# Kernel tuning notes

Hardware: AMD Instinct MI355X
Metric: run time of the kernel (lower is better)

Reference implementation:

```python
import jax, jax.numpy as jnp
import numpy as np

S, B, W, H = 97, 256, 1024, 16
HD = W // H


def setup_inputs() -> dict:
    key = jax.random.key(0)
    ks = jax.random.split(key, 16)
    def p(k, shape):
        return jax.random.normal(k, shape, jnp.float32) * 0.02
    return {
        "tensor": jax.random.normal(ks[0], (S, B, W), jnp.float32),
        "mask": jnp.zeros((S, S), jnp.float32),
        "q_w": p(ks[1], (W, W)), "q_b": p(ks[2], (W,)),
        "k_w": p(ks[3], (W, W)), "k_b": p(ks[4], (W,)),
        "v_w": p(ks[5], (W, W)), "v_b": p(ks[6], (W,)),
        "in_proj_w": p(ks[7], (3 * W, W)), "in_proj_b": p(ks[8], (3 * W,)),
        "mha_out_w": p(ks[9], (W, W)), "mha_out_b": p(ks[10], (W,)),
        "out_w": p(ks[11], (W, W)), "out_b": p(ks[12], (W,)),
    }


def _freqs_cos_sin(dim, seqlen, theta=10000.0):
    # matches precompute_freqs_cis: angle[t, j] = t / theta**(2j/dim)
    inv = 1.0 / (theta ** (jnp.arange(0, dim, 2, dtype=jnp.float32) / dim))  # (dim/2,)
    ang = jnp.arange(seqlen, dtype=jnp.float32)[:, None] * inv[None, :]      # (S, dim/2)
    return jnp.cos(ang)[:, None, :], jnp.sin(ang)[:, None, :]                # (S, 1, dim/2)


def _rotary(x, cos, sin):
    # x: (S, B, D); pairs (even, odd) along last dim form complex numbers
    s, b, d = x.shape
    xr = x.reshape(s, b, d // 2, 2)
    xe, xo = xr[..., 0], xr[..., 1]
    oe = xe * cos - xo * sin
    oo = xe * sin + xo * cos
    return jnp.stack([oe, oo], axis=-1).reshape(s, b, d)


def reference(tensor, mask, q_w, q_b, k_w, k_b, v_w, v_b,
              in_proj_w, in_proj_b, mha_out_w, mha_out_b, out_w, out_b):
    # tensor: (S, B, W) -- torch MHA default batch_first=False layout
    q = tensor @ q_w.T + q_b
    k = tensor @ k_w.T + k_b
    v = tensor @ v_w.T + v_b

    cos, sin = _freqs_cos_sin(W, S)
    q = _rotary(q, cos, sin)
    k = _rotary(k, cos, sin)

    # nn.MultiheadAttention internal in_proj (applied on top of q/k/v linears)
    Wq, Wk, Wv = in_proj_w[:W], in_proj_w[W:2 * W], in_proj_w[2 * W:]
    bq, bk, bv = in_proj_b[:W], in_proj_b[W:2 * W], in_proj_b[2 * W:]
    q = q @ Wq.T + bq
    k = k @ Wk.T + bk
    v = v @ Wv.T + bv

    def split_heads(x):  # (S,B,W) -> (B,H,S,HD)
        return x.reshape(S, B, H, HD).transpose(1, 2, 0, 3)

    qh, kh, vh = split_heads(q), split_heads(k), split_heads(v)
    scale = 1.0 / jnp.sqrt(jnp.float32(HD))
    scores = jnp.einsum('bhqd,bhkd->bhqk', qh, kh) * scale + mask  # additive float mask
    attn = jax.nn.softmax(scores, axis=-1)
    o = jnp.einsum('bhqk,bhkd->bhqd', attn, vh)      # (B,H,S,HD)
    o = o.transpose(2, 0, 1, 3).reshape(S, B, W)     # (S,B,W)
    o = o @ mha_out_w.T + mha_out_b                  # MHA out_proj
    return o @ out_w.T + out_b                       # module's final self.out
```

## Files before the change

### kernel.cpp

```cpp
#include <hip/hip_runtime.h>
#include <cstdint>
#include <cstddef>

#define S_LEN 97
#define B_DIM 256
#define W_DIM 1024
#define NH    16
#define HDIM  64
#define MROWS (S_LEN * B_DIM)

typedef unsigned short u16;
typedef __bf16 bf16x8 __attribute__((ext_vector_type(8)));
typedef float  f32x4  __attribute__((ext_vector_type(4)));

__device__ __forceinline__ u16 f2bf(float f) {
  __bf16 b = (__bf16)f;
  return __builtin_bit_cast(unsigned short, b);
}

__device__ __forceinline__ void gload16(const void* g, void* lds) {
  __builtin_amdgcn_global_load_lds(
      (const __attribute__((address_space(1))) void*)(uintptr_t)g,
      (__attribute__((address_space(3))) void*)(uint32_t)(uintptr_t)lds,
      16, 0, 0);
}

__global__ void k_prep(const float* __restrict__ tensor, u16* __restrict__ Xbf,
                       const float* __restrict__ q_w, const float* __restrict__ k_w,
                       const float* __restrict__ in_proj_w, const float* __restrict__ out_w,
                       u16* __restrict__ WC1, u16* __restrict__ W2, u16* __restrict__ WO,
                       const float* __restrict__ v_w, u16* __restrict__ WvT,
                       const float* __restrict__ mha_w, u16* __restrict__ WmT,
                       const float* __restrict__ v_b, const float* __restrict__ in_proj_b,
                       float* __restrict__ bvf,
                       const float* __restrict__ mha_b, const float* __restrict__ out_b,
                       float* __restrict__ bff,
                       float* __restrict__ tab, const float* __restrict__ mask,
                       float* __restrict__ maskP, const float* __restrict__ q_b,
                       const float* __restrict__ k_b, float* __restrict__ bc1,
                       float* __restrict__ zb) {
  __shared__ float tlds[32][33];
  const int blk = blockIdx.x, t = threadIdx.x;

  if (blk < 24832) {
    const int i = blk * 256 + t;
    float4 v = ((const float4*)tensor)[i];
    uint2 pk;
    pk.x = (uint32_t)f2bf(v.x) | ((uint32_t)f2bf(v.y) << 16);
    pk.y = (uint32_t)f2bf(v.z) | ((uint32_t)f2bf(v.w) << 16);
    ((uint2*)Xbf)[i] = pk;
  } else if (blk < 30976) {
    const int i = (blk - 24832) * 256 + t;
    const float* s; u16* d; int off;
    if (i < 262144)        { s = q_w;       d = WC1;           off = i; }
    else if (i < 524288)   { s = k_w;       d = WC1 + 1048576; off = i - 262144; }
    else if (i < 1310720)  { s = in_proj_w; d = W2;            off = i - 524288; }
    else                   { s = out_w;     d = WO;            off = i - 1310720; }
    float4 v = ((const float4*)s)[off];
    uint2 pk;
    pk.x = (uint32_t)f2bf(v.x) | ((uint32_t)f2bf(v.y) << 16);
    pk.y = (uint32_t)f2bf(v.z) | ((uint32_t)f2bf(v.w) << 16);
    ((uint2*)d)[off] = pk;
  } else if (blk < 33024) {
    const int idx = blk - 30976;
    const int z = idx >> 10, rem = idx & 1023;
    const float* src = z ? mha_w : v_w;
    u16* dst = z ? WmT : WvT;
    const int bx = (rem & 31) * 32, by = (rem >> 5) * 32;
    const int tx = t & 31, ty = t >> 5;
    for (int yy = ty; yy < 32; yy += 8)
      tlds[yy][tx] = src[(size_t)(by + yy) * 1024 + bx + tx];
    __syncthreads();
    for (int yy = ty; yy < 32; yy += 8)
      dst[(size_t)(bx + yy) * 1024 + by + tx] = f2bf(tlds[tx][yy]);
  } else if (blk < 33536) {
    const int bb = blk - 33024;
    const int lane = t & 63, wave = t >> 6;
    const float* M; const float* v; const float* b2; float* out; int rb;
    if (bb < 256) { M = in_proj_w + (size_t)2048 * 1024; v = v_b; b2 = in_proj_b + 2048; out = bvf; rb = bb * 4; }
    else          { M = out_w; v = mha_b; b2 = out_b; out = bff; rb = (bb - 256) * 4; }
    const int row = rb + wave;
    float s = 0.f;
    for (int k = lane; k < 1024; k += 64) s += M[(size_t)row * 1024 + k] * v[k];
#pragma unroll
    for (int d = 32; d; d >>= 1) s += __shfl_xor(s, d);
    if (lane == 0) out[row] = s + b2[row];
  } else {
    const int bb = blk - 33536;
    if (bb < 194) {
      const int idx = bb * 256 + t;
      if (idx < S_LEN * 512) {
        const int s = idx / 512, i = idx % 512;
        const float freq = expf(-(float)i * (9.210340371976184f / 512.0f));
        float sv, cv;
        sincosf((float)s * freq, &sv, &cv);
        tab[idx * 2 + 0] = cv;
        tab[idx * 2 + 1] = sv;
      }
    } else if (bb < 258) {
      const int i = (bb - 194) * 256 + t;
      const int r = i >> 7, c = i & 127;
      float v;
      if (c >= S_LEN) v = -1e30f;
      else if (r < S_LEN) v = mask[r * S_LEN + c];
      else v = 0.f;
      maskP[i] = v;
    } else if (bb < 266) {
      const int i = (bb - 258) * 256 + t;
      bc1[i] = (i < W_DIM) ? q_b[i] : k_b[i - W_DIM];
    } else {
      const int i = (bb - 266) * 256 + t;
      zb[i] = 0.f;
    }
  }
}

__global__ __launch_bounds__(256) void k_gemmfold(
    const u16* __restrict__ A0, const u16* __restrict__ B0, u16* __restrict__ C0,
    const u16* __restrict__ A1, const u16* __restrict__ B1, u16* __restrict__ C1,
    const float* __restrict__ zb) {
  __shared__ u16 As[128 * 64];
  __shared__ u16 Bs[128 * 64];

  const u16* A = blockIdx.z ? A1 : A0;
  const u16* Bw = blockIdx.z ? B1 : B0;
  u16* Cp = blockIdx.z ? C1 : C0;

  const int tid = threadIdx.x, lane = tid & 63, wave = tid >> 6;
  const int wm = wave >> 1, wn = wave & 1;
  const int m0 = blockIdx.y * 128;
  const int n0 = blockIdx.x * 128;

  f32x4 acc[4][4] = {};

  const int lrow = lane >> 3;
  const int lcol = (lane & 7) * 8;
  const u16* Ag = A + (size_t)(m0 + wave * 8 + lrow) * 1024 + lcol;
  const u16* Bg = Bw + (size_t)(n0 + wave * 8 + lrow) * 1024 + lcol;
  u16* Asl = As + wave * 8 * 64;
  u16* Bsl = Bs + wave * 8 * 64;

  for (int kt = 0; kt < 1024; kt += 64) {
#pragma unroll
    for (int i = 0; i < 4; ++i) {
      gload16(Ag + (size_t)(i * 32) * 1024 + kt, Asl + i * 2048);
      gload16(Bg + (size_t)(i * 32) * 1024 + kt, Bsl + i * 2048);
    }
    __syncthreads();
#pragma unroll
    for (int kk = 0; kk < 2; ++kk) {
      bf16x8 af[4], bfr[4];
#pragma unroll
      for (int m = 0; m < 4; ++m)
        af[m] = *(const bf16x8*)(As + (wm * 64 + m * 16 + (lane & 15)) * 64 + kk * 32 + (lane >> 4) * 8);
#pragma unroll
      for (int n = 0; n < 4; ++n)
        bfr[n] = *(const bf16x8*)(Bs + (wn * 64 + n * 16 + (lane & 15)) * 64 + kk * 32 + (lane >> 4) * 8);
#pragma unroll
      for (int m = 0; m < 4; ++m)
#pragma unroll
        for (int n = 0; n < 4; ++n)
          acc[m][n] = __builtin_amdgcn_mfma_f32_16x16x32_bf16(af[m], bfr[n], acc[m][n], 0, 0, 0);
    }
    __syncthreads();
  }

  const int r0 = (lane >> 4) * 4;
  const int c0 = lane & 15;
#pragma unroll
  for (int m = 0; m < 4; ++m)
#pragma unroll
    for (int n = 0; n < 4; ++n) {
      const int col = n0 + wn * 64 + n * 16 + c0;
#pragma unroll
      for (int r = 0; r < 4; ++r) {
        const int row = m0 + wm * 64 + m * 16 + r0 + r;
        Cp[(size_t)row * 1024 + col] = f2bf(acc[m][n][r] + zb[col]);
      }
    }
}

template <int MODE>
__global__ __launch_bounds__(512, 4) void k_gemm256(
    const u16* __restrict__ A, int lda,
    const u16* __restrict__ BwA, const u16* __restrict__ BwB,
    const float* __restrict__ biasA, const float* __restrict__ biasB,
    void* __restrict__ CpA, void* __restrict__ CpB, int ldc,
    size_t thirdStride, const float* __restrict__ tab, int Nt, int NtA) {
  __shared__ u16 lds[3 * 12288];

  const int tid = threadIdx.x, lane = tid & 63, wave = tid >> 6;
  const int wm = wave >> 2, wn = wave & 3;
  const int c0 = lane & 15, hi = lane >> 4;

  const int nwg = gridDim.x;
  const int qq = nwg >> 3, rr_ = nwg & 7;
  const int xcd = blockIdx.x & 7, sub = blockIdx.x >> 3;
  const int seq = (xcd < rr_ ? xcd * (qq + 1) : rr_ * (qq + 1) + (xcd - rr_) * qq) + sub;
  const int mt = seq / Nt, ntRaw = seq - mt * Nt;
  const int m0 = mt * 128;
  bool isV = false;
  int n0 = ntRaw * 256;
  const u16* Bbase;
  const float* bias;
  if (MODE == 0) {
    if (ntRaw >= NtA) {
      isV = true;
      n0 = (ntRaw - NtA) * 256;
      Bbase = BwB + (size_t)n0 * 1024;
      bias = biasB;
    } else {
      Bbase = BwA + (size_t)n0 * 1024;
      bias = biasA;
    }
  } else {
    Bbase = BwA + (size_t)n0 * 1024;
    bias = biasA;
  }
  const int aoff = (MODE == 1) ? (n0 & ~1023) : 0;

  const int Lb = tid >> 3, pc = tid & 7;
  const int lcl = pc ^ (Lb & 7);
  const int rsel = lcl >> 2;
  const int csel = (lcl & 3) * 8;
  const u16* aS = A + (size_t)(m0 + Lb + 64 * rsel) * lda + aoff + csel;
  const u16* bS0 = Bbase + (size_t)(Lb + 128 * rsel) * 1024 + csel;
  const u16* bS1 = Bbase + (size_t)(64 + Lb + 128 * rsel) * 1024 + csel;
  const uint32_t ldsW = wave * 512;

  auto stage = [&](int tt, u16* slot) {
    gload16(aS + tt * 32, slot + ldsW);
    gload16(bS0 + tt * 32, slot + 4096 + ldsW);
    gload16(bS1 + tt * 32, slot + 8192 + ldsW);
  };

  int aofr[4], bofr[4];
#pragma unroll
  for (int m = 0; m < 4; ++m)
    aofr[m] = (m * 16 + c0) * 64 + ((((wm << 2) | hi) ^ (c0 & 7)) * 8);
#pragma unroll
  for (int n = 0; n < 4; ++n)
    bofr[n] = 4096 + ((wn & 1) * 64 + n * 16 + c0) * 64 +
              (((((wn >> 1) << 2) | hi) ^ (c0 & 7)) * 8);

  u16* s0 = lds;
  u16* s1 = lds + 12288;
  u16* s2 = lds + 24576;

  stage(0, s0); stage(1, s1);
  asm volatile("s_waitcnt vmcnt(3)" ::: "memory");
  __builtin_amdgcn_s_barrier();
  __builtin_amdgcn_sched_barrier(0);

  f32x4 acc[4][4] = {};

  for (int t = 0; t < 32; ++t) {
    bf16x8 af[4], bfr[4];
#pragma unroll
    for (int n = 0; n < 4; ++n) bfr[n] = *(const bf16x8*)(s0 + bofr[n]);
#pragma unroll
    for (int m = 0; m < 4; ++m) af[m] = *(const bf16x8*)(s0 + aofr[m]);
    if (t + 2 < 32) stage(t + 2, s2);
    __builtin_amdgcn_s_setprio(1);
#pragma unroll
    for (int m = 0; m < 4; ++m)
#pragma unroll
      for (int n = 0; n < 4; ++n)
        acc[m][n] = __builtin_amdgcn_mfma_f32_16x16x32_bf16(af[m], bfr[n], acc[m][n], 0, 0, 0);
    __builtin_amdgcn_s_setprio(0);
    if (t < 31) {
      if (t < 30) asm volatile("s_waitcnt vmcnt(3)" ::: "memory");
      else        asm volatile("s_waitcnt vmcnt(0)" ::: "memory");
      __builtin_amdgcn_s_barrier();
      __builtin_amdgcn_sched_barrier(0);
      u16* tmp = s0; s0 = s1; s1 = s2; s2 = tmp;
    }
  }

  const int r0 = (lane >> 4) * 4;
#pragma unroll
  for (int m = 0; m < 4; ++m) {
#pragma unroll
    for (int n = 0; n < 4; ++n) {
      const int col = n0 + wn * 64 + n * 16 + c0;
      const float bv = bias[col];
      if (MODE == 0 && !isV) {
        const int pairI = (col & 1023) >> 1;
        const float sgn = (col & 1) ? 1.f : -1.f;
#pragma unroll
        for (int r = 0; r < 4; ++r) {
          const int row = m0 + wm * 64 + m * 16 + r0 + r;
          const float v = acc[m][n][r] + bv;
          const float p = __shfl_xor(v, 1);
          const float2 cs = ((const float2*)tab)[(row >> 8) * 512 + pairI];
          ((u16*)CpA)[(size_t)row * ldc + col] = f2bf(v * cs.x + sgn * p * cs.y);
        }
      } else if (MODE == 0 && isV) {
        const int h = (col >> 6) & 15, d = col & 63;
#pragma unroll
        for (int r = 0; r < 4; ++r) {
          const int row = m0 + wm * 64 + m * 16 + r0 + r;
          const int s = row >> 8, b = row & 255;
          ((u16*)CpB)[(((size_t)(b * NH + h) * S_LEN + s) * HDIM + d)] =
              f2bf(acc[m][n][r] + bv);
        }
      } else if (MODE == 1) {
        const int which = col >> 10, c = col & 1023;
        const int h = c >> 6, d = c & 63;
        const float sc = (which == 0) ? 0.125f : 1.0f;
#pragma unroll
        for (int r = 0; r < 4; ++r) {
          const int row = m0 + wm * 64 + m * 16 + r0 + r;
          const int s = row >> 8, b = row & 255;
          ((u16*)CpA)[(size_t)which * thirdStride +
                      (((size_t)(b * NH + h) * S_LEN + s) * HDIM + d)] =
              f2bf((acc[m][n][r] + bv) * sc);
        }
      } else {
#pragma unroll
        for (int r = 0; r < 4; ++r) {
          const int row = m0 + wm * 64 + m * 16 + r0 + r;
          ((float*)CpA)[(size_t)row * ldc + col] = acc[m][n][r] + bv;
        }
      }
    }
  }
}

__global__ __launch_bounds__(512, 6) void k_attn(const u16* __restrict__ qkv2,
                                                 const float* __restrict__ maskP,
                                                 u16* __restrict__ O1) {
  __shared__ u16 Vt[64 * 128];
  __shared__ u16 Pb[128 * 128];
  __shared__ float redS[4][128];

  const size_t TS = (size_t)MROWS * W_DIM;
  const int bh = blockIdx.x, b = bh >> 4, h = bh & 15;
  const int tid = threadIdx.x, lane = tid & 63, wave = tid >> 6;
  const int wm = wave >> 2;
  const int wn = wave & 3;
  const int c0 = lane & 15, hi = lane >> 4;

  const u16* Qg = qkv2 + (size_t)bh * (S_LEN * HDIM);
  const u16* Kg = Qg + TS;
  const u16* Vg = Qg + 2 * TS;

  for (int idx = tid; idx < 1024; idx += 512) {
    const int s = idx >> 3, c = (idx & 7) * 8;
    uint4 vv = make_uint4(0, 0, 0, 0);
    if (s < S_LEN) vv = *(const uint4*)(Vg + (size_t)s * HDIM + c);
    u16 tmp[8];
    *(uint4*)tmp = vv;
#pragma unroll
    for (int j = 0; j < 8; ++j)
      Vt[(c + j) * 128 + (s ^ (j << 3))] = tmp[j];
  }

  f32x4 acc[4][2] = {};
#pragma unroll
  for (int kk = 0; kk < 2; ++kk) {
    bf16x8 af[4], bfr[2];
#pragma unroll
    for (int m = 0; m < 4; ++m)
      af[m] = *(const bf16x8*)(Qg + (size_t)(wm * 64 + m * 16 + c0) * HDIM + kk * 32 + hi * 8);
#pragma unroll
    for (int n = 0; n < 2; ++n)
      bfr[n] = *(const bf16x8*)(Kg + (size_t)(wn * 32 + n * 16 + c0) * HDIM + kk * 32 + hi * 8);
#pragma unroll
    for (int m = 0; m < 4; ++m)
#pragma unroll
      for (int n = 0; n < 2; ++n)
        acc[m][n] = __builtin_amdgcn_mfma_f32_16x16x32_bf16(af[m], bfr[n], acc[m][n], 0, 0, 0);
  }

#pragma unroll
  for (int m = 0; m < 4; ++m) {
    float psm[4];
#pragma unroll
    for (int r = 0; r < 4; ++r) {
      const int row = wm * 64 + m * 16 + hi * 4 + r;
      float p = 0.f;
#pragma unroll
      for (int n = 0; n < 2; ++n) {
        const int col = wn * 32 + n * 16 + c0;
        const float e = __expf(acc[m][n][r] + maskP[row * 128 + col]);
        p += e;
        Pb[row * 128 + (col ^ ((row & 7) << 3))] = f2bf(e);
      }
      psm[r] = p;
    }
#pragma unroll
    for (int d = 1; d < 16; d <<= 1)
#pragma unroll
      for (int r = 0; r < 4; ++r)
        psm[r] += __shfl_xor(psm[r], d);
    if (c0 == 0) {
#pragma unroll
      for (int r = 0; r < 4; ++r)
        redS[wn][wm * 64 + m * 16 + hi * 4 + r] = psm[r];
    }
  }
  __syncthreads();

  f32x4 o[4] = {};
#pragma unroll
  for (int kk = 0; kk < 4; ++kk) {
    bf16x8 pa[4], vb;
#pragma unroll
    for (int m = 0; m < 4; ++m) {
      const int row = wm * 64 + m * 16 + c0;
      pa[m] = *(const bf16x8*)(Pb + row * 128 + ((kk * 32 + hi * 8) ^ ((row & 7) << 3)));
    }
    {
      const int d = wn * 16 + c0;
      vb = *(const bf16x8*)(Vt + d * 128 + ((kk * 32 + hi * 8) ^ ((d & 7) << 3)));
    }
#pragma unroll
    for (int m = 0; m < 4; ++m)
      o[m] = __builtin_amdgcn_mfma_f32_16x16x32_bf16(pa[m], vb, o[m], 0, 0, 0);
  }
  __syncthreads();

  u16* Ob = Pb;
#pragma unroll
  for (int m = 0; m < 4; ++m)
#pragma unroll
    for (int r = 0; r < 4; ++r) {
      const int row = wm * 64 + m * 16 + hi * 4 + r;
      const float iv = 1.0f / (redS[0][row] + redS[1][row] + redS[2][row] + redS[3][row]);
      Ob[row * 80 + wn * 16 + c0] = f2bf(o[m][r] * iv);
    }
  __syncthreads();

  if (tid < 4 * S_LEN) {
    const int row = tid >> 2, q = tid & 3;
    const u16* src = Ob + row * 80 + q * 16;
    uint4 a0 = *(const uint4*)(src);
    uint4 a1 = *(const uint4*)(src + 8);
    u16* dst = O1 + ((size_t)row * B_DIM + b) * W_DIM + h * HDIM + q * 16;
    *(uint4*)dst = a0;
    *(uint4*)(dst + 8) = a1;
  }
}

extern "C" void kernel_launch(void* const* d_in, const int* in_sizes, int n_in,
                              void* d_out, int out_size, void* d_ws, size_t ws_size,
                              hipStream_t stream) {
  (void)in_sizes; (void)n_in; (void)out_size; (void)ws_size;
  const float* tensor    = (const float*)d_in[0];
  const float* mask      = (const float*)d_in[1];
  const float* q_w       = (const float*)d_in[2];
  const float* q_b       = (const float*)d_in[3];
  const float* k_w       = (const float*)d_in[4];
  const float* k_b       = (const float*)d_in[5];
  const float* v_w       = (const float*)d_in[6];
  const float* v_b       = (const float*)d_in[7];
  const float* in_proj_w = (const float*)d_in[8];
  const float* in_proj_b = (const float*)d_in[9];
  const float* mha_w     = (const float*)d_in[10];
  const float* mha_b     = (const float*)d_in[11];
  const float* out_w     = (const float*)d_in[12];
  const float* out_b     = (const float*)d_in[13];

  char* ws = (char*)d_ws;
  size_t off = 0;
  auto alloc = [&](size_t bytes) {
    char* p = ws + off;
    off += (bytes + 255) & ~(size_t)255;
    return p;
  };

  const size_t TS = (size_t)MROWS * W_DIM;

  float* tab = (float*)alloc((size_t)S_LEN * 512 * 2 * sizeof(float));
  float* maskP = (float*)alloc((size_t)128 * 128 * sizeof(float));
  u16* Xbf   = (u16*)alloc(TS * 2);
  u16* qkv1  = (u16*)alloc((size_t)MROWS * 2048 * 2);
  u16* qkv2  = (u16*)alloc(TS * 3 * 2);
  u16* WC1   = (u16*)alloc((size_t)2048 * 1024 * 2);
  u16* W2    = (u16*)alloc((size_t)3072 * 1024 * 2);
  u16* WvT   = (u16*)alloc((size_t)1024 * 1024 * 2);
  u16* WmT   = (u16*)alloc((size_t)1024 * 1024 * 2);
  u16* WO    = (u16*)alloc((size_t)1024 * 1024 * 2);
  u16* WVf   = (u16*)alloc((size_t)1024 * 1024 * 2);
  u16* WFf   = (u16*)alloc((size_t)1024 * 1024 * 2);
  float* bc1 = (float*)alloc(2048 * sizeof(float));
  float* bvf = (float*)alloc(1024 * sizeof(float));
  float* bff = (float*)alloc(1024 * sizeof(float));
  float* zb  = (float*)alloc(1024 * sizeof(float));
  u16* O1 = Xbf;

  k_prep<<<dim3(33806), 256, 0, stream>>>(
      tensor, Xbf, q_w, k_w, in_proj_w, out_w, WC1, W2, WO,
      v_w, WvT, mha_w, WmT, v_b, in_proj_b, bvf, mha_b, out_b, bff,
      tab, mask, maskP, q_b, k_b, bc1, zb);

  k_gemmfold<<<dim3(8, 8, 2), 256, 0, stream>>>(
      W2 + (size_t)2048 * 1024, WvT, WVf, WO, WmT, WFf, zb);

  k_gemm256<0><<<dim3(194 * 12), 512, 0, stream>>>(
      Xbf, W_DIM, WC1, WVf, bc1, bvf, qkv1, qkv2 + 2 * TS, 2048, TS, tab, 12, 8);

  k_gemm256<1><<<dim3(194 * 8), 512, 0, stream>>>(
      qkv1, 2048, W2, nullptr, in_proj_b, nullptr, qkv2, nullptr, 0, TS, nullptr, 8, 0);

  k_attn<<<dim3(B_DIM * NH), 512, 0, stream>>>(qkv2, maskP, O1);

  k_gemm256<2><<<dim3(194 * 4), 512, 0, stream>>>(
      O1, W_DIM, WFf, nullptr, bff, nullptr, d_out, nullptr, W_DIM, 0, nullptr, 4, 0);
}
```

Baseline: 523.4 us.

## Compute softmax row sums via MFMA with a ones column; prefetch mask

The attention kernel drops the shuffle-based row-sum reduction of the exponentials and the four-way cross-wave sum. Instead it appends a row of bf16 ones to the transposed V tile and has one wave column compute the row sums with extra MFMAs against P. Mask values are loaded into registers at kernel start so their latency overlaps the V staging, and the occupancy hint drops from 6 to 4. Sums now come from the bf16-rounded P values, which keeps them consistent with the numerator but adds MFMA work on wave column 0 and raises register pressure.

```diff
diff --git a/kernel.cpp b/kernel.cpp
--- a/kernel.cpp
+++ b/kernel.cpp
@@ -327,12 +327,12 @@
   }
 }
 
-__global__ __launch_bounds__(512, 6) void k_attn(const u16* __restrict__ qkv2,
+__global__ __launch_bounds__(512, 4) void k_attn(const u16* __restrict__ qkv2,
                                                  const float* __restrict__ maskP,
                                                  u16* __restrict__ O1) {
-  __shared__ u16 Vt[64 * 128];
+  __shared__ u16 Vt[66 * 128];
   __shared__ u16 Pb[128 * 128];
-  __shared__ float redS[4][128];
+  __shared__ float redS[128];
 
   const size_t TS = (size_t)MROWS * W_DIM;
   const int bh = blockIdx.x, b = bh >> 4, h = bh & 15;
@@ -345,6 +345,15 @@
   const u16* Kg = Qg + TS;
   const u16* Vg = Qg + 2 * TS;
 
+  float mk[4][2][4];
+#pragma unroll
+  for (int m = 0; m < 4; ++m)
+#pragma unroll
+    for (int n = 0; n < 2; ++n)
+#pragma unroll
+      for (int r = 0; r < 4; ++r)
+        mk[m][n][r] = maskP[(wm * 64 + m * 16 + hi * 4 + r) * 128 + wn * 32 + n * 16 + c0];
+
   for (int idx = tid; idx < 1024; idx += 512) {
     const int s = idx >> 3, c = (idx & 7) * 8;
     uint4 vv = make_uint4(0, 0, 0, 0);
@@ -355,6 +364,7 @@
     for (int j = 0; j < 8; ++j)
       Vt[(c + j) * 128 + (s ^ (j << 3))] = tmp[j];
   }
+  if (tid < 128) Vt[64 * 128 + tid] = 0x3F80;
 
   f32x4 acc[4][2] = {};
 #pragma unroll
@@ -375,37 +385,24 @@
 
 #pragma unroll
   for (int m = 0; m < 4; ++m) {
-    float psm[4];
 #pragma unroll
     for (int r = 0; r < 4; ++r) {
       const int row = wm * 64 + m * 16 + hi * 4 + r;
-      float p = 0.f;
 #pragma unroll
       for (int n = 0; n < 2; ++n) {
         const int col = wn * 32 + n * 16 + c0;
-        const float e = __expf(acc[m][n][r] + maskP[row * 128 + col]);
-        p += e;
+        const float e = __expf(acc[m][n][r] + mk[m][n][r]);
         Pb[row * 128 + (col ^ ((row & 7) << 3))] = f2bf(e);
       }
-      psm[r] = p;
-    }
-#pragma unroll
-    for (int d = 1; d < 16; d <<= 1)
-#pragma unroll
-      for (int r = 0; r < 4; ++r)
-        psm[r] += __shfl_xor(psm[r], d);
-    if (c0 == 0) {
-#pragma unroll
-      for (int r = 0; r < 4; ++r)
-        redS[wn][wm * 64 + m * 16 + hi * 4 + r] = psm[r];
     }
   }
   __syncthreads();
 
   f32x4 o[4] = {};
+  f32x4 osum[4] = {};
 #pragma unroll
   for (int kk = 0; kk < 4; ++kk) {
-    bf16x8 pa[4], vb;
+    bf16x8 pa[4], vb, vbs;
 #pragma unroll
     for (int m = 0; m < 4; ++m) {
       const int row = wm * 64 + m * 16 + c0;
@@ -415,9 +412,24 @@
       const int d = wn * 16 + c0;
       vb = *(const bf16x8*)(Vt + d * 128 + ((kk * 32 + hi * 8) ^ ((d & 7) << 3)));
     }
+    if (wn == 0)
+      vbs = *(const bf16x8*)(Vt + 64 * 128 + (kk * 32 + hi * 8));
 #pragma unroll
     for (int m = 0; m < 4; ++m)
       o[m] = __builtin_amdgcn_mfma_f32_16x16x32_bf16(pa[m], vb, o[m], 0, 0, 0);
+    if (wn == 0) {
+#pragma unroll
+      for (int m = 0; m < 4; ++m)
+        osum[m] = __builtin_amdgcn_mfma_f32_16x16x32_bf16(pa[m], vbs, osum[m], 0, 0, 0);
+    }
+  }
+
+  if (wn == 0 && c0 == 0) {
+#pragma unroll
+    for (int m = 0; m < 4; ++m)
+#pragma unroll
+      for (int r = 0; r < 4; ++r)
+        redS[wm * 64 + m * 16 + hi * 4 + r] = osum[m][r];
   }
   __syncthreads();
 
@@ -427,7 +439,7 @@
 #pragma unroll
     for (int r = 0; r < 4; ++r) {
       const int row = wm * 64 + m * 16 + hi * 4 + r;
-      const float iv = 1.0f / (redS[0][row] + redS[1][row] + redS[2][row] + redS[3][row]);
+      const float iv = 1.0f / redS[row];
       Ob[row * 80 + wn * 16 + c0] = f2bf(o[m][r] * iv);
     }
   __syncthreads();
```

Result: faster. 509.2 us, median of 2 (-2.7%).
